# Kernel tuning notes

Hardware: AMD Instinct MI355X
Metric: run time of the kernel (lower is better)

Reference implementation:

```python
import jax, jax.numpy as jnp
import numpy as np

N_NODES = 100000
N_EDGES = 1600000
IN_DIM = 8
EMB = 50
NUM_TASK = 112
NUM_LAYER = 2
BN_EPS = 1e-5


def setup_inputs() -> dict:
    key = jax.random.key(0)
    ks = jax.random.split(key, 12)
    s = 0.1  # weight init scale
    L, D = NUM_LAYER, EMB
    return {
        "src": jax.random.randint(ks[0], (N_EDGES,), 0, N_NODES),
        "dst": jax.random.randint(ks[1], (N_EDGES,), 0, N_NODES),
        "node_feats": jax.random.normal(ks[2], (N_NODES, IN_DIM), jnp.float32),
        "edge_feats": jax.random.normal(ks[3], (N_EDGES, IN_DIM), jnp.float32),
        "node_W": jax.random.normal(ks[4], (IN_DIM, D), jnp.float32) * s,
        "node_b": jnp.zeros((D,), jnp.float32),
        "edge_W": jax.random.normal(ks[5], (IN_DIM, D), jnp.float32) * s,
        "edge_b": jnp.zeros((D,), jnp.float32),
        "eps": jnp.zeros((L,), jnp.float32),
        "W1": jax.random.normal(ks[6], (L, D, 2 * D), jnp.float32) * s,
        "b1": jnp.zeros((L, 2 * D), jnp.float32),
        "g1": jnp.ones((L, 2 * D), jnp.float32),
        "be1": jnp.zeros((L, 2 * D), jnp.float32),
        "W2": jax.random.normal(ks[7], (L, 2 * D, D), jnp.float32) * s,
        "b2": jnp.zeros((L, D), jnp.float32),
        "g2": jnp.ones((L, D), jnp.float32),
        "be2": jnp.zeros((L, D), jnp.float32),
        "pred_W": jax.random.normal(ks[8], (D, NUM_TASK), jnp.float32) * s,
        "pred_b": jnp.zeros((NUM_TASK,), jnp.float32),
    }


def _bn(x, gamma, beta):
    # BatchNorm1d in training mode: batch mean, biased variance, eps=1e-5
    mu = jnp.mean(x, axis=0)
    var = jnp.mean(jnp.square(x - mu), axis=0)
    return (x - mu) * jax.lax.rsqrt(var + BN_EPS) * gamma + beta


def reference(src, dst, node_feats, edge_feats, node_W, node_b, edge_W, edge_b,
              eps, W1, b1, g1, be1, W2, b2, g2, be2, pred_W, pred_b):
    N = node_feats.shape[0]
    h = node_feats @ node_W + node_b          # [N, D] node encoder
    e = edge_feats @ edge_W + edge_b          # [E, D] edge encoder
    deg = jax.ops.segment_sum(jnp.ones(src.shape, h.dtype), dst, num_segments=N)
    inv_deg = jnp.where(deg > 0, 1.0 / jnp.maximum(deg, 1.0), 0.0)[:, None]  # mean; 0 for isolated nodes
    for i in range(W1.shape[0]):
        m = h[src] + e                                          # u_add_e
        agg = jax.ops.segment_sum(m, dst, num_segments=N) * inv_deg  # mean reduce
        h = (1.0 + eps[i]) * h + agg                            # eps-combine
        h = jax.nn.relu(_bn(h @ W1[i] + b1[i], g1[i], be1[i]))
        h = jax.nn.relu(_bn(h @ W2[i] + b2[i], g2[i], be2[i]))
    return h @ pred_W + pred_b                # [N, num_task]
```

## Files before the change

### kernel.cpp

```cpp
#include <hip/hip_runtime.h>
#include <hip/hip_bf16.h>

#define N_NODES 100000
#define N_EDGES 1600000
#define IN_DIM 8
#define D 50
#define D2 100
#define NTASK 112
#define BN_EPS 1e-5f
#define NBLK ((N_NODES + 255) / 256)
#define HS 56
#define SLOT 48

#define PARTS 8
#define NPP (N_NODES / PARTS)
#define SF_BPP 128
typedef int i4 __attribute__((ext_vector_type(4)));
typedef __attribute__((ext_vector_type(8))) short s16x8;
typedef __attribute__((ext_vector_type(4))) float f32x4;

__device__ __forceinline__ unsigned bf16_rn(float x) {
    unsigned u = __float_as_uint(x);
    return (u + 0x7fffu + ((u >> 16) & 1u)) >> 16;
}
__device__ __forceinline__ unsigned pack_bf16(float a, float b) {
    return bf16_rn(a) | (bf16_rn(b) << 16);
}

__global__ __launch_bounds__(256) void node_enc_pair(
    const float* __restrict__ nf, const float* __restrict__ nW,
    const float* __restrict__ nb, float* __restrict__ h,
    unsigned* __restrict__ hb) {
    __shared__ float sW[IN_DIM * D];
    __shared__ float sb[D];
    __shared__ float snf[10 * IN_DIM];
    int t = threadIdx.x;
    int n0 = blockIdx.x * 10;
    for (int i = t; i < IN_DIM * D; i += 256) sW[i] = nW[i];
    for (int i = t; i < D; i += 256) sb[i] = nb[i];
    for (int i = t; i < 10 * IN_DIM; i += 256) {
        int g = n0 * IN_DIM + i;
        snf[i] = (g < N_NODES * IN_DIM) ? nf[g] : 0.0f;
    }
    __syncthreads();
    if (t >= 250) return;
    int n = t / 25, j2 = t % 25;
    int g = n0 + n;
    if (g >= N_NODES) return;
    int j0 = 2 * j2, j1 = j0 + 1;
    float v0 = sb[j0], v1 = sb[j1];
#pragma unroll
    for (int k = 0; k < IN_DIM; k++) {
        float f = snf[n * IN_DIM + k];
        v0 += f * sW[k * D + j0];
        v1 += f * sW[k * D + j1];
    }
    *(float2*)&h[(size_t)g * HS + j0] = make_float2(v0, v1);
    if (hb) hb[(size_t)g * 32 + j2] = pack_bf16(v0, v1);
}

__global__ __launch_bounds__(256) void k_slotfill_part(
    const int* __restrict__ src, const int* __restrict__ dst,
    int* __restrict__ degi, int2* __restrict__ slots) {
    const int part = blockIdx.x & (PARTS - 1);
    const int blk = blockIdx.x >> 3;
    const int lo = part * NPP, hi = lo + NPP;
    const int NT = SF_BPP * 256;
    const int NG = N_EDGES / 4;
    const i4* s4 = (const i4*)src;
    const i4* d4 = (const i4*)dst;
    for (int g = blk * 256 + (int)threadIdx.x; g < NG; g += NT) {
        i4 dd = __builtin_nontemporal_load(d4 + g);
        i4 ss = __builtin_nontemporal_load(s4 + g);
#pragma unroll
        for (int k = 0; k < 4; k++) {
            int d = dd[k];
            if (d >= lo && d < hi) {
                int pos = atomicAdd(&degi[d], 1);
                if (pos < SLOT) slots[(size_t)d * SLOT + pos] = make_int2(ss[k], 4 * g + k);
            }
        }
    }
}

__global__ __launch_bounds__(256) void k_aggef_slot(
    const int* __restrict__ degi, const int2* __restrict__ slots,
    const float* __restrict__ ef, float* __restrict__ aggef) {
    int lane = threadIdx.x & 63, wv = threadIdx.x >> 6;
    int n = (blockIdx.x & 7) * NPP + (blockIdx.x >> 3) * 4 + wv;
    if (n >= N_NODES) return;
    int deg = degi[n];
    if (deg > SLOT) deg = SLOT;
    int g = lane >> 3, k = lane & 7;
    float a = 0.0f;
    for (int q = g; q < deg; q += 8) {
        int e = slots[(size_t)n * SLOT + q].y;
        a += ef[(size_t)e * 8 + k];
    }
    a += __shfl_xor(a, 8, 64);
    a += __shfl_xor(a, 16, 64);
    a += __shfl_xor(a, 32, 64);
    if (lane < 8) aggef[(size_t)n * 8 + lane] = a;
}

template<bool USE_HB>
__global__ __launch_bounds__(256) void gather_slot(
    const int* __restrict__ degi, const int2* __restrict__ slots,
    const float* __restrict__ aggef, const float* __restrict__ eW,
    const float* __restrict__ eb, const float* __restrict__ h,
    const unsigned* __restrict__ hb, const float* __restrict__ epsArr,
    int layer, float* __restrict__ hnew) {
    __shared__ float sW[IN_DIM * D];
    __shared__ float sB[D];
    int t = threadIdx.x;
    for (int i = t; i < IN_DIM * D; i += 256) sW[i] = eW[i];
    for (int i = t; i < D; i += 256) sB[i] = eb[i];
    __syncthreads();
    int lane = t & 63, wv = t >> 6, half = lane >> 5, li = lane & 31;
    int part = blockIdx.x & 7, bi = blockIdx.x >> 3;
    int r = bi * 8 + wv * 2 + half;
    if (r >= NPP) return;
    int n = part * NPP + r;
    int deg = degi[n];
    if (deg > SLOT) deg = SLOT;
    float iv = (deg > 0) ? (1.0f / (float)deg) : 0.0f;
    const int2* srow = &slots[(size_t)n * SLOT];
    float ax0 = 0, ay0 = 0, ax1 = 0, ay1 = 0;
    for (int p = 0; p < deg; p += 4) {
        int4 q0 = *(const int4*)&srow[p];
        int4 q1 = *(const int4*)&srow[p + 2];
        if (li < 25) {
            if (USE_HB) {
                unsigned w = hb[(size_t)q0.x * 32 + li];
                ax0 += __uint_as_float(w << 16);
                ay0 += __uint_as_float(w & 0xffff0000u);
                if (p + 1 < deg) {
                    w = hb[(size_t)q0.z * 32 + li];
                    ax1 += __uint_as_float(w << 16);
                    ay1 += __uint_as_float(w & 0xffff0000u);
                }
                if (p + 2 < deg) {
                    w = hb[(size_t)q1.x * 32 + li];
                    ax0 += __uint_as_float(w << 16);
                    ay0 += __uint_as_float(w & 0xffff0000u);
                }
                if (p + 3 < deg) {
                    w = hb[(size_t)q1.z * 32 + li];
                    ax1 += __uint_as_float(w << 16);
                    ay1 += __uint_as_float(w & 0xffff0000u);
                }
            } else {
                float2 v = *(const float2*)&h[(size_t)q0.x * HS + 2 * li];
                ax0 += v.x; ay0 += v.y;
                if (p + 1 < deg) {
                    v = *(const float2*)&h[(size_t)q0.z * HS + 2 * li];
                    ax1 += v.x; ay1 += v.y;
                }
                if (p + 2 < deg) {
                    v = *(const float2*)&h[(size_t)q1.x * HS + 2 * li];
                    ax0 += v.x; ay0 += v.y;
                }
                if (p + 3 < deg) {
                    v = *(const float2*)&h[(size_t)q1.z * HS + 2 * li];
                    ax1 += v.x; ay1 += v.y;
                }
            }
        }
    }
    if (li < 25) {
        float accx = ax0 + ax1, accy = ay0 + ay1;
        int j0 = 2 * li, j1 = j0 + 1;
        float e0 = 0.0f, e1 = 0.0f;
        if (deg > 0) {
            const float* ag = &aggef[(size_t)n * 8];
            float s0 = 0.0f, s1 = 0.0f;
#pragma unroll
            for (int k = 0; k < 8; k++) {
                float a = ag[k];
                s0 += a * sW[k * D + j0];
                s1 += a * sW[k * D + j1];
            }
            e0 = s0 * iv + sB[j0];
            e1 = s1 * iv + sB[j1];
        }
        float epsv = 1.0f + epsArr[layer];
        float2 hv = *(const float2*)&h[(size_t)n * HS + j0];
        float2 o;
        o.x = epsv * hv.x + iv * accx + e0;
        o.y = epsv * hv.y + iv * accy + e1;
        *(float2*)&hnew[(size_t)n * D + j0] = o;
    }
}

template<int K, int KP, int J, int JP, bool BN_IN, bool STATS>
__global__ __launch_bounds__(256) void gemm_mfma(
    const float* __restrict__ X, const float* __restrict__ W,
    const float* __restrict__ bias,
    const float* __restrict__ bnS, const float* __restrict__ bnQ,
    const float* __restrict__ bnG, const float* __restrict__ bnB,
    float* __restrict__ Y, float* __restrict__ sg, float* __restrict__ qg,
    int ntiles) {
    constexpr int RB = 64;
    constexpr int WS = KP + 8;
    constexpr int KS = KP / 32;
    constexpr int NCT = JP / 16;
    constexpr bool RAGGED = (N_NODES % RB) != 0;
    __shared__ __align__(16) unsigned short shA_hi[RB * WS];
    __shared__ __align__(16) unsigned short shA_lo[RB * WS];
    __shared__ __align__(16) unsigned short sWT_hi[JP * WS];
    __shared__ __align__(16) unsigned short sWT_lo[JP * WS];
    __shared__ float sb[JP];
    __shared__ float sa[BN_IN ? K : 1], sc[BN_IN ? K : 1];
    __shared__ float sp[JP], qp[JP];
    int t = threadIdx.x;
    for (int i = t; i < RB * WS; i += 256) { shA_hi[i] = 0; shA_lo[i] = 0; }
    for (int i = t; i < JP * WS; i += 256) { sWT_hi[i] = 0; sWT_lo[i] = 0; }
    __syncthreads();
    for (int i = t; i < KP * JP; i += 256) {
        int k = i / JP, j = i % JP;
        float v = (k < K && j < J) ? W[k * J + j] : 0.0f;
        unsigned hv = bf16_rn(v);
        float hf = __uint_as_float(hv << 16);
        sWT_hi[j * WS + k] = (unsigned short)hv;
        sWT_lo[j * WS + k] = (unsigned short)bf16_rn(v - hf);
    }
    for (int i = t; i < JP; i += 256) sb[i] = (i < J) ? bias[i] : 0.0f;
    if (BN_IN) {
        const float invN = 1.0f / (float)N_NODES;
        for (int i = t; i < K; i += 256) {
            float mu = bnS[i] * invN;
            float var = bnQ[i] * invN - mu * mu;
            float rs = rsqrtf(var + BN_EPS);
            float a = bnG[i] * rs;
            sa[i] = a;
            sc[i] = bnB[i] - mu * a;
        }
    }
    if (STATS) {
        for (int i = t; i < JP; i += 256) { sp[i] = 0.0f; qp[i] = 0.0f; }
    }
    int lane = t & 63, wv = t >> 6;
    int lrow = lane & 15, lkg = lane >> 4;
    float sacc[NCT], qacc[NCT];
#pragma unroll
    for (int c = 0; c < NCT; c++) { sacc[c] = 0.0f; qacc[c] = 0.0f; }
    for (int tile = blockIdx.x; tile < ntiles; tile += gridDim.x) {
        __syncthreads();
        int base = tile * RB;
        for (int i = t; i < RB * K; i += 256) {
            int r = i / K, k = i % K;
            float v = 0.0f;
            if (!RAGGED || base + r < N_NODES) {
                v = X[(size_t)base * K + i];
                if (BN_IN) v = fmaxf(v * sa[k] + sc[k], 0.0f);
            }
            unsigned hv = bf16_rn(v);
            float hf = __uint_as_float(hv << 16);
            shA_hi[r * WS + k] = (unsigned short)hv;
            shA_lo[r * WS + k] = (unsigned short)bf16_rn(v - hf);
        }
        __syncthreads();
        s16x8 ah[KS], al[KS];
        int arow = wv * 16 + lrow;
#pragma unroll
        for (int ks = 0; ks < KS; ks++) {
            int off = arow * WS + ks * 32 + lkg * 8;
            ah[ks] = *(const s16x8*)&shA_hi[off];
            al[ks] = *(const s16x8*)&shA_lo[off];
        }
#pragma unroll
        for (int ct = 0; ct < NCT; ct++) {
            f32x4 a0 = {0.f, 0.f, 0.f, 0.f};
            f32x4 a1 = {0.f, 0.f, 0.f, 0.f};
            f32x4 a2 = {0.f, 0.f, 0.f, 0.f};
#pragma unroll
            for (int ks = 0; ks < KS; ks++) {
                int boff = (ct * 16 + lrow) * WS + ks * 32 + lkg * 8;
                s16x8 bh = *(const s16x8*)&sWT_hi[boff];
                s16x8 bl = *(const s16x8*)&sWT_lo[boff];
                a0 = __builtin_amdgcn_mfma_f32_16x16x32_bf16(ah[ks], bh, a0, 0, 0, 0);
                a1 = __builtin_amdgcn_mfma_f32_16x16x32_bf16(ah[ks], bl, a1, 0, 0, 0);
                a2 = __builtin_amdgcn_mfma_f32_16x16x32_bf16(al[ks], bh, a2, 0, 0, 0);
            }
            int col = ct * 16 + lrow;
#pragma unroll
            for (int j = 0; j < 4; j++) {
                int gn = base + wv * 16 + lkg * 4 + j;
                if (!RAGGED || gn < N_NODES) {
                    float v = a0[j] + (a1[j] + a2[j]) + sb[col];
                    if (col < J) Y[(size_t)gn * J + col] = v;
                    if (STATS) { sacc[ct] += v; qacc[ct] += v * v; }
                }
            }
        }
    }
    if (STATS) {
        __syncthreads();
#pragma unroll
        for (int c = 0; c < NCT; c++) {
            atomicAdd(&sp[c * 16 + (t & 15)], sacc[c]);
            atomicAdd(&qp[c * 16 + (t & 15)], qacc[c]);
        }
        __syncthreads();
        for (int i = t; i < J; i += 256) {
            atomicAdd(&sg[i], sp[i]);
            atomicAdd(&qg[i], qp[i]);
        }
    }
}

__global__ __launch_bounds__(256) void apply2_pair(
    const float* __restrict__ y2, const float* __restrict__ sr,
    const float* __restrict__ qr, const float* __restrict__ g,
    const float* __restrict__ be, float* __restrict__ h,
    unsigned* __restrict__ hb) {
    __shared__ float sa[D], sc[D];
    int t = threadIdx.x;
    if (t < D) {
        float invN = 1.0f / (float)N_NODES;
        float mu = sr[t] * invN;
        float var = qr[t] * invN - mu * mu;
        float rs = rsqrtf(var + BN_EPS);
        float a = g[t] * rs;
        sa[t] = a;
        sc[t] = be[t] - mu * a;
    }
    __syncthreads();
    int idx = blockIdx.x * 256 + t;
    if (idx >= N_NODES * 25) return;
    int n = idx / 25, j2 = idx % 25;
    int j0 = 2 * j2, j1 = j0 + 1;
    float2 y = *(const float2*)&y2[(size_t)n * D + j0];
    float v0 = fmaxf(y.x * sa[j0] + sc[j0], 0.0f);
    float v1 = fmaxf(y.y * sa[j1] + sc[j1], 0.0f);
    *(float2*)&h[(size_t)n * HS + j0] = make_float2(v0, v1);
    if (hb) hb[(size_t)n * 32 + j2] = pack_bf16(v0, v1);
}

__global__ void k_deg(const int* __restrict__ dst, int* __restrict__ degi) {
    int e = blockIdx.x * blockDim.x + threadIdx.x;
    if (e < N_EDGES) atomicAdd(&degi[dst[e]], 1);
}
__global__ void k_bsum(const int* __restrict__ degi, int* __restrict__ bsum) {
    __shared__ int lds[256];
    int t = threadIdx.x, i = blockIdx.x * 256 + t;
    lds[t] = (i < N_NODES) ? degi[i] : 0;
    __syncthreads();
    for (int s = 128; s > 0; s >>= 1) {
        if (t < s) lds[t] += lds[t + s];
        __syncthreads();
    }
    if (t == 0) bsum[blockIdx.x] = lds[0];
}
__global__ void k_bscan(const int* __restrict__ bsum, int* __restrict__ bpre) {
    __shared__ int lds[512];
    int t = threadIdx.x;
    int x = (t < NBLK) ? bsum[t] : 0;
    lds[t] = x;
    __syncthreads();
    int acc = x;
    for (int s = 1; s < 512; s <<= 1) {
        int add = (t >= s) ? lds[t - s] : 0;
        __syncthreads();
        acc += add;
        lds[t] = acc;
        __syncthreads();
    }
    if (t < NBLK) bpre[t] = acc - x;
}
__global__ void k_off(int* __restrict__ degi, const int* __restrict__ bpre,
                      int* __restrict__ off, float* __restrict__ invd) {
    __shared__ int lds[256];
    int t = threadIdx.x, i = blockIdx.x * 256 + t;
    int dv = (i < N_NODES) ? degi[i] : 0;
    lds[t] = dv;
    __syncthreads();
    int acc = dv;
    for (int s = 1; s < 256; s <<= 1) {
        int add = (t >= s) ? lds[t - s] : 0;
        __syncthreads();
        acc += add;
        lds[t] = acc;
        __syncthreads();
    }
    int excl = acc - dv + bpre[blockIdx.x];
    if (i < N_NODES) {
        off[i] = excl;
        degi[i] = excl;
        invd[i] = (dv > 0) ? (1.0f / (float)dv) : 0.0f;
    }
    if (i == 0) off[N_NODES] = N_EDGES;
}
__global__ void k_fill(const int* __restrict__ src, const int* __restrict__ dst,
                       int* __restrict__ cursor, int2* __restrict__ adj) {
    int e = blockIdx.x * blockDim.x + threadIdx.x;
    if (e >= N_EDGES) return;
    int d = dst[e];
    int pos = atomicAdd(&cursor[d], 1);
    adj[pos] = make_int2(src[e], e);
}
__global__ __launch_bounds__(256) void k_aggef_csr(
    const int* __restrict__ off, const int2* __restrict__ adj,
    const float* __restrict__ ef, float* __restrict__ aggef) {
    int lane = threadIdx.x & 63, wv = threadIdx.x >> 6;
    int n = blockIdx.x * 4 + wv;
    if (n >= N_NODES) return;
    int p0 = off[n], pend = off[n + 1];
    int g = lane >> 3, k = lane & 7;
    float a = 0.0f;
    for (int q = p0 + g; q < pend; q += 8) a += ef[(size_t)adj[q].y * 8 + k];
    a += __shfl_xor(a, 8, 64);
    a += __shfl_xor(a, 16, 64);
    a += __shfl_xor(a, 32, 64);
    if (lane < 8) aggef[(size_t)n * 8 + lane] = a;
}
__global__ __launch_bounds__(256) void gather_csr(
    const int* __restrict__ off, const int2* __restrict__ adj,
    const float* __restrict__ aggef, const float* __restrict__ eW,
    const float* __restrict__ eb, const float* __restrict__ h,
    const float* __restrict__ invd, const float* __restrict__ epsArr,
    int layer, float* __restrict__ hnew) {
    __shared__ float sW[IN_DIM * D];
    __shared__ float sB[D];
    int t = threadIdx.x;
    for (int i = t; i < IN_DIM * D; i += 256) sW[i] = eW[i];
    for (int i = t; i < D; i += 256) sB[i] = eb[i];
    __syncthreads();
    int lane = t & 63, wv = t >> 6;
    int n = blockIdx.x * 4 + wv;
    if (n >= N_NODES) return;
    int dd = (lane < D) ? lane : (D - 1);
    int p = off[n], pend = off[n + 1];
    int deg = pend - p;
    float acc = 0.0f;
    while (p + 4 <= pend) {
        int s0 = adj[p].x, s1 = adj[p + 1].x, s2 = adj[p + 2].x, s3 = adj[p + 3].x;
        acc += h[(size_t)s0 * HS + dd] + h[(size_t)s1 * HS + dd]
             + h[(size_t)s2 * HS + dd] + h[(size_t)s3 * HS + dd];
        p += 4;
    }
    while (p < pend) { acc += h[(size_t)adj[p].x * HS + dd]; p++; }
    if (lane < D) {
        float iv = invd[n];
        float extra = 0.0f;
        if (deg > 0) {
            const float* ag = &aggef[(size_t)n * 8];
            float s = 0.0f;
#pragma unroll
            for (int k = 0; k < 8; k++) s += ag[k] * sW[k * D + dd];
            extra = s * iv + sB[dd];
        }
        float epsv = 1.0f + epsArr[layer];
        hnew[(size_t)n * D + lane] = epsv * h[(size_t)n * HS + lane] + iv * acc + extra;
    }
}

extern "C" void kernel_launch(void* const* d_in, const int* in_sizes, int n_in,
                              void* d_out, int out_size, void* d_ws, size_t ws_size,
                              hipStream_t stream) {
    const int*   src        = (const int*)d_in[0];
    const int*   dst        = (const int*)d_in[1];
    const float* node_feats = (const float*)d_in[2];
    const float* edge_feats = (const float*)d_in[3];
    const float* node_W     = (const float*)d_in[4];
    const float* node_b     = (const float*)d_in[5];
    const float* edge_W     = (const float*)d_in[6];
    const float* edge_b     = (const float*)d_in[7];
    const float* epsArr     = (const float*)d_in[8];
    const float* W1         = (const float*)d_in[9];
    const float* b1         = (const float*)d_in[10];
    const float* g1         = (const float*)d_in[11];
    const float* be1        = (const float*)d_in[12];
    const float* W2         = (const float*)d_in[13];
    const float* b2         = (const float*)d_in[14];
    const float* g2         = (const float*)d_in[15];
    const float* be2        = (const float*)d_in[16];
    const float* pred_W     = (const float*)d_in[17];
    const float* pred_b     = (const float*)d_in[18];
    float* out = (float*)d_out;

    float* ws = (float*)d_ws;
    unsigned* hb = nullptr;
    float *h, *tmp, *invd = nullptr, *st, *aggef;
    int *degi, *off = nullptr, *bsum = nullptr, *bpre = nullptr;
    int2 *slots = nullptr, *adj = nullptr;

    auto layout = [&](int mode) -> size_t {
        float* p = ws;
        hb = nullptr; slots = nullptr; adj = nullptr;
        off = nullptr; bsum = nullptr; bpre = nullptr; invd = nullptr;
        if (mode == 2) { hb = (unsigned*)p; p += (size_t)N_NODES * 32; }
        h = p;    p += (size_t)N_NODES * HS;
        tmp = p;  p += (size_t)N_NODES * D;
        st = p;   p += 768;
        if (mode == 0) { invd = p; p += N_NODES; }
        int* ip = (int*)p;
        degi = ip; ip += N_NODES;
        char* end;
        if (mode >= 1) {
            slots = (int2*)ip;
            aggef = (float*)(slots + (size_t)N_NODES * SLOT);
            end = (char*)(aggef + (size_t)N_NODES * 8);
        } else {
            off = ip;  ip += N_NODES + 1;
            bsum = ip; ip += NBLK;
            bpre = ip; ip += NBLK + 1;
            adj = (int2*)ip;
            aggef = (float*)(adj + N_EDGES);
            end = (char*)(aggef + (size_t)N_NODES * 8);
        }
        return (size_t)(end - (char*)d_ws);
    };
    int mode = 2;
    if (ws_size < layout(2)) { mode = 1; if (ws_size < layout(1)) { mode = 0; layout(0); } }

    float* s1 = st, *q1 = st + 128, *s2 = st + 256, *q2 = st + 320;
    float* y1 = out;

    node_enc_pair<<<10000, 256, 0, stream>>>(node_feats, node_W, node_b, h, hb);
    hipMemsetAsync(degi, 0, N_NODES * sizeof(int), stream);

    const int GATHER_GRID = PARTS * ((NPP + 7) / 8);
    if (mode >= 1) {
        k_slotfill_part<<<PARTS * SF_BPP, 256, 0, stream>>>(src, dst, degi, slots);
        k_aggef_slot<<<(N_NODES + 3) / 4, 256, 0, stream>>>(degi, slots, edge_feats, aggef);
    } else {
        k_deg<<<(N_EDGES + 255) / 256, 256, 0, stream>>>(dst, degi);
        k_bsum<<<NBLK, 256, 0, stream>>>(degi, bsum);
        k_bscan<<<1, 512, 0, stream>>>(bsum, bpre);
        k_off<<<NBLK, 256, 0, stream>>>(degi, bpre, off, invd);
        k_fill<<<(N_EDGES + 255) / 256, 256, 0, stream>>>(src, dst, degi, adj);
        k_aggef_csr<<<(N_NODES + 3) / 4, 256, 0, stream>>>(off, adj, edge_feats, aggef);
    }

    const int NT64 = (N_NODES + 63) / 64;
    for (int layer = 0; layer < 2; layer++) {
        hipMemsetAsync(st, 0, 384 * sizeof(float), stream);
        if (mode == 2)
            gather_slot<true><<<GATHER_GRID, 256, 0, stream>>>(
                degi, slots, aggef, edge_W, edge_b, h, hb, epsArr, layer, tmp);
        else if (mode == 1)
            gather_slot<false><<<GATHER_GRID, 256, 0, stream>>>(
                degi, slots, aggef, edge_W, edge_b, h, nullptr, epsArr, layer, tmp);
        else
            gather_csr<<<(N_NODES + 3) / 4, 256, 0, stream>>>(
                off, adj, aggef, edge_W, edge_b, h, invd, epsArr, layer, tmp);
        gemm_mfma<50, 64, 100, 112, false, true><<<768, 256, 0, stream>>>(
            tmp, W1 + layer * D * D2, b1 + layer * D2, st, st, st, st, y1, s1, q1, NT64);
        gemm_mfma<100, 128, 50, 64, true, true><<<512, 256, 0, stream>>>(
            y1, W2 + layer * D2 * D, b2 + layer * D,
            s1, q1, g1 + layer * D2, be1 + layer * D2, tmp, s2, q2, NT64);
        if (layer == 0)
            apply2_pair<<<(N_NODES * 25 + 255) / 256, 256, 0, stream>>>(
                tmp, s2, q2, g2, be2, h, hb);
    }
    gemm_mfma<50, 64, 112, 112, true, false><<<768, 256, 0, stream>>>(
        tmp, pred_W, pred_b, s2, q2, g2 + D, be2 + D, out, st, st, NT64);
}
```

Baseline: 713.1 us.

## Fuse edge-feature aggregation into slot fill with atomics and shrink slots to int

Removes the separate per-node edge-feature aggregation kernel by having the slot-fill kernel atomically add each edge's 8 features into the destination node's aggregate, after zeroing it with a memset. Slots now store only the source index (int instead of int2), which halves slot memory and the index traffic in the gather. The bf16 gather loop is unrolled by 8 with vectorized index loads. The cost is 8 float atomics per edge, and the feature sums now depend on atomic ordering; the fused kernel also sums edges beyond SLOT that the old version dropped.

Result: slower. 1.260 ms (+76.7%).

```diff
diff --git a/kernel.cpp b/kernel.cpp
--- a/kernel.cpp
+++ b/kernel.cpp
@@ -61,7 +61,9 @@
 
 __global__ __launch_bounds__(256) void k_slotfill_part(
     const int* __restrict__ src, const int* __restrict__ dst,
-    int* __restrict__ degi, int2* __restrict__ slots) {
+    const float* __restrict__ ef,
+    int* __restrict__ degi, int* __restrict__ slots,
+    float* __restrict__ aggef) {
     const int part = blockIdx.x & (PARTS - 1);
     const int blk = blockIdx.x >> 3;
     const int lo = part * NPP, hi = lo + NPP;
@@ -77,35 +79,22 @@
             int d = dd[k];
             if (d >= lo && d < hi) {
                 int pos = atomicAdd(&degi[d], 1);
-                if (pos < SLOT) slots[(size_t)d * SLOT + pos] = make_int2(ss[k], 4 * g + k);
-            }
-        }
-    }
-}
-
-__global__ __launch_bounds__(256) void k_aggef_slot(
-    const int* __restrict__ degi, const int2* __restrict__ slots,
-    const float* __restrict__ ef, float* __restrict__ aggef) {
-    int lane = threadIdx.x & 63, wv = threadIdx.x >> 6;
-    int n = (blockIdx.x & 7) * NPP + (blockIdx.x >> 3) * 4 + wv;
-    if (n >= N_NODES) return;
-    int deg = degi[n];
-    if (deg > SLOT) deg = SLOT;
-    int g = lane >> 3, k = lane & 7;
-    float a = 0.0f;
-    for (int q = g; q < deg; q += 8) {
-        int e = slots[(size_t)n * SLOT + q].y;
-        a += ef[(size_t)e * 8 + k];
-    }
-    a += __shfl_xor(a, 8, 64);
-    a += __shfl_xor(a, 16, 64);
-    a += __shfl_xor(a, 32, 64);
-    if (lane < 8) aggef[(size_t)n * 8 + lane] = a;
+                if (pos < SLOT) slots[(size_t)d * SLOT + pos] = ss[k];
+                const float4* er = (const float4*)&ef[(size_t)(4 * g + k) * 8];
+                float4 ea = er[0], eb4 = er[1];
+                float* ag = &aggef[(size_t)d * 8];
+                atomicAdd(ag + 0, ea.x);  atomicAdd(ag + 1, ea.y);
+                atomicAdd(ag + 2, ea.z);  atomicAdd(ag + 3, ea.w);
+                atomicAdd(ag + 4, eb4.x); atomicAdd(ag + 5, eb4.y);
+                atomicAdd(ag + 6, eb4.z); atomicAdd(ag + 7, eb4.w);
+            }
+        }
+    }
 }
 
 template<bool USE_HB>
 __global__ __launch_bounds__(256) void gather_slot(
-    const int* __restrict__ degi, const int2* __restrict__ slots,
+    const int* __restrict__ degi, const int* __restrict__ slots,
     const float* __restrict__ aggef, const float* __restrict__ eW,
     const float* __restrict__ eb, const float* __restrict__ h,
     const unsigned* __restrict__ hb, const float* __restrict__ epsArr,
@@ -124,44 +113,55 @@
     int deg = degi[n];
     if (deg > SLOT) deg = SLOT;
     float iv = (deg > 0) ? (1.0f / (float)deg) : 0.0f;
-    const int2* srow = &slots[(size_t)n * SLOT];
+    const int* srow = &slots[(size_t)n * SLOT];
     float ax0 = 0, ay0 = 0, ax1 = 0, ay1 = 0;
-    for (int p = 0; p < deg; p += 4) {
-        int4 q0 = *(const int4*)&srow[p];
-        int4 q1 = *(const int4*)&srow[p + 2];
-        if (li < 25) {
-            if (USE_HB) {
-                unsigned w = hb[(size_t)q0.x * 32 + li];
-                ax0 += __uint_as_float(w << 16);
-                ay0 += __uint_as_float(w & 0xffff0000u);
-                if (p + 1 < deg) {
-                    w = hb[(size_t)q0.z * 32 + li];
-                    ax1 += __uint_as_float(w << 16);
-                    ay1 += __uint_as_float(w & 0xffff0000u);
-                }
-                if (p + 2 < deg) {
-                    w = hb[(size_t)q1.x * 32 + li];
-                    ax0 += __uint_as_float(w << 16);
-                    ay0 += __uint_as_float(w & 0xffff0000u);
-                }
-                if (p + 3 < deg) {
-                    w = hb[(size_t)q1.z * 32 + li];
-                    ax1 += __uint_as_float(w << 16);
-                    ay1 += __uint_as_float(w & 0xffff0000u);
-                }
-            } else {
-                float2 v = *(const float2*)&h[(size_t)q0.x * HS + 2 * li];
+    int p = 0;
+    if (USE_HB) {
+        for (; p + 8 <= deg; p += 8) {
+            i4 s0 = *(const i4*)&srow[p];
+            i4 s1 = *(const i4*)&srow[p + 4];
+            if (li < 25) {
+                unsigned w;
+                w = hb[(size_t)s0[0] * 32 + li]; ax0 += __uint_as_float(w << 16); ay0 += __uint_as_float(w & 0xffff0000u);
+                w = hb[(size_t)s0[1] * 32 + li]; ax1 += __uint_as_float(w << 16); ay1 += __uint_as_float(w & 0xffff0000u);
+                w = hb[(size_t)s0[2] * 32 + li]; ax0 += __uint_as_float(w << 16); ay0 += __uint_as_float(w & 0xffff0000u);
+                w = hb[(size_t)s0[3] * 32 + li]; ax1 += __uint_as_float(w << 16); ay1 += __uint_as_float(w & 0xffff0000u);
+                w = hb[(size_t)s1[0] * 32 + li]; ax0 += __uint_as_float(w << 16); ay0 += __uint_as_float(w & 0xffff0000u);
+                w = hb[(size_t)s1[1] * 32 + li]; ax1 += __uint_as_float(w << 16); ay1 += __uint_as_float(w & 0xffff0000u);
+                w = hb[(size_t)s1[2] * 32 + li]; ax0 += __uint_as_float(w << 16); ay0 += __uint_as_float(w & 0xffff0000u);
+                w = hb[(size_t)s1[3] * 32 + li]; ax1 += __uint_as_float(w << 16); ay1 += __uint_as_float(w & 0xffff0000u);
+            }
+        }
+        if (p < deg) {
+            i4 s0 = *(const i4*)&srow[p];
+            i4 s1 = *(const i4*)&srow[p + 4];
+            if (li < 25) {
+                unsigned w;
+                w = hb[(size_t)s0[0] * 32 + li]; ax0 += __uint_as_float(w << 16); ay0 += __uint_as_float(w & 0xffff0000u);
+                if (p + 1 < deg) { w = hb[(size_t)s0[1] * 32 + li]; ax1 += __uint_as_float(w << 16); ay1 += __uint_as_float(w & 0xffff0000u); }
+                if (p + 2 < deg) { w = hb[(size_t)s0[2] * 32 + li]; ax0 += __uint_as_float(w << 16); ay0 += __uint_as_float(w & 0xffff0000u); }
+                if (p + 3 < deg) { w = hb[(size_t)s0[3] * 32 + li]; ax1 += __uint_as_float(w << 16); ay1 += __uint_as_float(w & 0xffff0000u); }
+                if (p + 4 < deg) { w = hb[(size_t)s1[0] * 32 + li]; ax0 += __uint_as_float(w << 16); ay0 += __uint_as_float(w & 0xffff0000u); }
+                if (p + 5 < deg) { w = hb[(size_t)s1[1] * 32 + li]; ax1 += __uint_as_float(w << 16); ay1 += __uint_as_float(w & 0xffff0000u); }
+                if (p + 6 < deg) { w = hb[(size_t)s1[2] * 32 + li]; ax0 += __uint_as_float(w << 16); ay0 += __uint_as_float(w & 0xffff0000u); }
+            }
+        }
+    } else {
+        for (; p < deg; p += 4) {
+            i4 s0 = *(const i4*)&srow[p];
+            if (li < 25) {
+                float2 v = *(const float2*)&h[(size_t)s0[0] * HS + 2 * li];
                 ax0 += v.x; ay0 += v.y;
                 if (p + 1 < deg) {
-                    v = *(const float2*)&h[(size_t)q0.z * HS + 2 * li];
+                    v = *(const float2*)&h[(size_t)s0[1] * HS + 2 * li];
                     ax1 += v.x; ay1 += v.y;
                 }
                 if (p + 2 < deg) {
-                    v = *(const float2*)&h[(size_t)q1.x * HS + 2 * li];
+                    v = *(const float2*)&h[(size_t)s0[2] * HS + 2 * li];
                     ax0 += v.x; ay0 += v.y;
                 }
                 if (p + 3 < deg) {
-                    v = *(const float2*)&h[(size_t)q1.z * HS + 2 * li];
+                    v = *(const float2*)&h[(size_t)s0[3] * HS + 2 * li];
                     ax1 += v.x; ay1 += v.y;
                 }
             }
@@ -483,7 +483,8 @@
     unsigned* hb = nullptr;
     float *h, *tmp, *invd = nullptr, *st, *aggef;
     int *degi, *off = nullptr, *bsum = nullptr, *bpre = nullptr;
-    int2 *slots = nullptr, *adj = nullptr;
+    int *slots = nullptr;
+    int2 *adj = nullptr;
 
     auto layout = [&](int mode) -> size_t {
         float* p = ws;
@@ -498,7 +499,7 @@
         degi = ip; ip += N_NODES;
         char* end;
         if (mode >= 1) {
-            slots = (int2*)ip;
+            slots = ip;
             aggef = (float*)(slots + (size_t)N_NODES * SLOT);
             end = (char*)(aggef + (size_t)N_NODES * 8);
         } else {
@@ -522,8 +523,9 @@
 
     const int GATHER_GRID = PARTS * ((NPP + 7) / 8);
     if (mode >= 1) {
-        k_slotfill_part<<<PARTS * SF_BPP, 256, 0, stream>>>(src, dst, degi, slots);
-        k_aggef_slot<<<(N_NODES + 3) / 4, 256, 0, stream>>>(degi, slots, edge_feats, aggef);
+        hipMemsetAsync(aggef, 0, (size_t)N_NODES * 8 * sizeof(float), stream);
+        k_slotfill_part<<<PARTS * SF_BPP, 256, 0, stream>>>(
+            src, dst, edge_feats, degi, slots, aggef);
     } else {
         k_deg<<<(N_EDGES + 255) / 256, 256, 0, stream>>>(dst, degi);
         k_bsum<<<NBLK, 256, 0, stream>>>(degi, bsum);
```
